# Kernel tuning notes

Measured on AMD Instinct MI355X. Metric: run time of the kernel, lower is better.

The kernel has to match this reference:

```python
import jax, jax.numpy as jnp
import numpy as np

B, S, D, DS = 8, 2048, 1024, 128
TEMP = 1.0
C = 8.0


def setup_inputs() -> dict:
    key = jax.random.key(0)
    ks = jax.random.split(key, 8)
    s_in = 1.0 / np.sqrt(D)
    s_st = 1.0 / np.sqrt(DS)
    return {
        "x": jax.random.normal(ks[0], (B, S, D), jnp.float32),
        "W_k": jax.random.normal(ks[1], (DS, D), jnp.float32) * s_in,
        "W_v": jax.random.normal(ks[2], (DS, D), jnp.float32) * s_in,
        "W_q": jax.random.normal(ks[3], (DS, D), jnp.float32) * s_in,
        "W_alpha_w": jax.random.normal(ks[4], (DS, D), jnp.float32) * s_in,
        "W_alpha_b": jnp.zeros((DS,), jnp.float32),
        "lambda_param": jax.random.uniform(ks[5], (DS,), jnp.float32, 4.0, 9.0),
        "W_o": jax.random.normal(ks[6], (D, DS), jnp.float32) * s_st,
        "norm_weight": jnp.ones((DS,), jnp.float32),
    }


def _l2norm(z):
    # matches F.normalize(..., dim=-1) with eps=1e-12
    n = jnp.linalg.norm(z, axis=-1, keepdims=True)
    return z / jnp.maximum(n, 1e-12)


def reference(x, W_k, W_v, W_q, W_alpha_w, W_alpha_b, lambda_param, W_o, norm_weight):
    # projections
    k = _l2norm(x @ W_k.T)                      # [B,S,DS]
    v = x @ W_v.T                               # [B,S,DS]
    q = _l2norm(x @ W_q.T)                      # [B,S,DS]
    r = jax.nn.sigmoid(x @ W_alpha_w.T + W_alpha_b)
    log_a = jnp.log(jax.nn.sigmoid(lambda_param) + 1e-8)  # [DS]
    alpha = jnp.exp(C * r * log_a)              # [B,S,DS], data-dependent decay

    H0 = jnp.zeros((B, DS, DS), x.dtype)        # state indexed [b, k, v]

    def step(H, inp):
        k_t, v_t, q_t, a_t = inp                # each [B,DS]
        # surprise: prediction error against current state
        pred = jnp.einsum('bk,bkv->bv', q_t, H)
        err = jnp.sum((v_t - pred) ** 2, axis=-1, keepdims=True)  # [B,1]
        sur = jax.nn.sigmoid(err / (TEMP + 1e-6))                 # [B,1]
        # delta rule: k (x) v - k (x) (k^T H) = k (x) (v - k^T H)
        k_proj = jnp.einsum('bk,bkv->bv', k_t, H)
        delta = k_t[:, :, None] * (v_t - k_proj)[:, None, :]      # [B,DS,DS]
        a_e = a_t[:, :, None]                                     # decay on k-axis
        H = a_e * H + (1.0 - a_e) * (sur[:, :, None] * delta)
        y = jnp.einsum('bk,bkv->bv', q_t, H)
        return H, y

    seq = (k.transpose(1, 0, 2), v.transpose(1, 0, 2),
           q.transpose(1, 0, 2), alpha.transpose(1, 0, 2))
    _, ys = jax.lax.scan(step, H0, seq)         # ys: [S,B,DS]
    y = ys.transpose(1, 0, 2)                   # [B,S,DS]

    # RMSNorm (computed in fp32, like the torch module)
    yf = y.astype(jnp.float32)
    yn = yf * jax.lax.rsqrt(jnp.mean(yf * yf, axis=-1, keepdims=True) + 1e-6)
    yn = (yn * norm_weight).astype(y.dtype)
    return yn @ W_o.T                           # [B,S,D]
```

## Files before the change

### kernel.cpp

```cpp
#include <hip/hip_runtime.h>
#include <math.h>

#define S_LEN 2048
#define B_SZ 8
#define D_IN 1024
#define DS_ 128
#define INV_TEMP (1.0f/1.000001f)

__global__ __launch_bounds__(256) void proj_gemm(
    const float* __restrict__ X,
    const float* __restrict__ Wk, const float* __restrict__ Wv,
    const float* __restrict__ Wq, const float* __restrict__ Wa,
    float* __restrict__ P)
{
    __shared__ __align__(16) float As[32][68];
    __shared__ __align__(16) float Bs[32][68];
    const int tid = threadIdx.x;
    const int m0 = blockIdx.x * 64;
    const int n0 = blockIdx.y * 64;
    const int lr = tid >> 3;
    const int lk4 = tid & 7;

    const float* wrows[2];
#pragma unroll
    for (int i = 0; i < 2; i++) {
        int nn = n0 + lr + i * 32;
        const float* w;
        if      (nn < 128) w = Wk + (size_t)nn * D_IN;
        else if (nn < 256) w = Wv + (size_t)(nn - 128) * D_IN;
        else if (nn < 384) w = Wq + (size_t)(nn - 256) * D_IN;
        else               w = Wa + (size_t)(nn - 384) * D_IN;
        wrows[i] = w;
    }
    const int ty = tid >> 4, tx = tid & 15;
    float acc[4][4];
#pragma unroll
    for (int i = 0; i < 4; i++)
#pragma unroll
        for (int j = 0; j < 4; j++) acc[i][j] = 0.f;

    for (int k0 = 0; k0 < D_IN; k0 += 32) {
#pragma unroll
        for (int i = 0; i < 2; i++) {
            int m = lr + i * 32;
            float4 a4 = *(const float4*)(X + (size_t)(m0 + m) * D_IN + k0 + lk4 * 4);
            As[lk4*4+0][m] = a4.x; As[lk4*4+1][m] = a4.y;
            As[lk4*4+2][m] = a4.z; As[lk4*4+3][m] = a4.w;
            float4 b4 = *(const float4*)(wrows[i] + k0 + lk4 * 4);
            Bs[lk4*4+0][m] = b4.x; Bs[lk4*4+1][m] = b4.y;
            Bs[lk4*4+2][m] = b4.z; Bs[lk4*4+3][m] = b4.w;
        }
        __syncthreads();
#pragma unroll
        for (int kk = 0; kk < 32; kk++) {
            float4 a4 = *(const float4*)(&As[kk][ty * 4]);
            float4 b4 = *(const float4*)(&Bs[kk][tx * 4]);
            float a[4] = {a4.x, a4.y, a4.z, a4.w};
            float b[4] = {b4.x, b4.y, b4.z, b4.w};
#pragma unroll
            for (int i = 0; i < 4; i++)
#pragma unroll
                for (int j = 0; j < 4; j++)
                    acc[i][j] = fmaf(a[i], b[j], acc[i][j]);
        }
        __syncthreads();
    }
#pragma unroll
    for (int i = 0; i < 4; i++) {
        float4 o; o.x = acc[i][0]; o.y = acc[i][1]; o.z = acc[i][2]; o.w = acc[i][3];
        *(float4*)(P + (size_t)(m0 + ty * 4 + i) * 512 + n0 + tx * 4) = o;
    }
}

__global__ __launch_bounds__(128) void postproc(
    float* __restrict__ P, const float* __restrict__ bA, const float* __restrict__ lam)
{
    const int tok = blockIdx.x, i = threadIdx.x;
    float* row = P + (size_t)tok * 512;
    float kr = row[i], qr = row[256 + i], rr = row[384 + i];
    float ks = kr * kr, qs = qr * qr;
#pragma unroll
    for (int m = 1; m < 64; m <<= 1) { ks += __shfl_xor(ks, m); qs += __shfl_xor(qs, m); }
    __shared__ float sb[4];
    if ((i & 63) == 0) { sb[(i >> 6) * 2] = ks; sb[(i >> 6) * 2 + 1] = qs; }
    __syncthreads();
    float kn = sqrtf(sb[0] + sb[2]);
    float qn = sqrtf(sb[1] + sb[3]);
    float kinv = 1.0f / fmaxf(kn, 1e-12f);
    float qinv = 1.0f / fmaxf(qn, 1e-12f);
    float sr = 1.0f / (1.0f + __expf(-(rr + bA[i])));
    float sl = 1.0f / (1.0f + __expf(-lam[i]));
    float la = logf(sl + 1e-8f);
    row[i]       = kr * kinv;
    row[256 + i] = qr * qinv;
    row[384 + i] = __expf(8.0f * sr * la);
}

__global__ __launch_bounds__(256) void recurrence(
    const float* __restrict__ P, float* __restrict__ Y)
{
    const int b = blockIdx.x;
    const int tid = threadIdx.x;
    const int c = tid & 3;
    const int vp = tid >> 2;
    const int lane = tid & 63;
    const int wave = tid >> 6;

    __shared__ __align__(16) float Pbuf[3][576];
    __shared__ float errw[2][4];

    const float* Pb = P + (size_t)b * S_LEN * 512;
    float* Yb = Y + (size_t)b * S_LEN * DS_;

    float H0[32], H1[32];
#pragma unroll
    for (int j = 0; j < 32; j++) { H0[j] = 0.f; H1[j] = 0.f; }

    for (int i = tid; i < 3 * 576; i += 256) (&Pbuf[0][0])[i] = 0.f;
    __syncthreads();
    {
        float2 v2 = *(const float2*)(Pb + tid * 2);
        int i0 = tid * 2, i1 = i0 + 1;
        Pbuf[0][(i0 >> 7) * 144 + ((i0 >> 5) & 3) * 36 + (i0 & 31)] = v2.x;
        Pbuf[0][(i1 >> 7) * 144 + ((i1 >> 5) & 3) * 36 + (i1 & 31)] = v2.y;
    }
    __syncthreads();

    const int voff = 144 + (vp >> 4) * 36 + ((2 * vp) & 31);

#define DOT_STEP(u, comp) { float h0 = H0[j4*4+u], h1 = H1[j4*4+u]; \
    pr0 = fmaf(q4.comp, h0, pr0); pr1 = fmaf(q4.comp, h1, pr1); \
    kp0 = fmaf(k4.comp, h0, kp0); kp1 = fmaf(k4.comp, h1, kp1); \
    yp0 = fmaf(p4.comp, h0, yp0); yp1 = fmaf(p4.comp, h1, yp1); }

#define UPD_STEP(u, comp) { float t0 = k4.comp * sd0, t1 = k4.comp * sd1; \
    H0[j4*4+u] = fmaf(a4.comp, H0[j4*4+u] - t0, t0); \
    H1[j4*4+u] = fmaf(a4.comp, H1[j4*4+u] - t1, t1); }

    for (int t = 0; t < S_LEN; t++) {
        const int pc = t % 3, pn = (t + 1) % 3, pp = (t + 2) % 3;
        const float* bq = &Pbuf[pc][2 * 144 + c * 36];
        const float* bk = &Pbuf[pc][c * 36];
        const float* bp = &Pbuf[pp][2 * 144 + c * 36];
        float pr0 = 0, pr1 = 0, kp0 = 0, kp1 = 0, yp0 = 0, yp1 = 0;
#pragma unroll
        for (int j4 = 0; j4 < 8; j4++) {
            float4 q4 = *(const float4*)(bq + j4 * 4);
            float4 k4 = *(const float4*)(bk + j4 * 4);
            float4 p4 = *(const float4*)(bp + j4 * 4);
            DOT_STEP(0, x) DOT_STEP(1, y) DOT_STEP(2, z) DOT_STEP(3, w)
        }
#pragma unroll
        for (int m = 1; m <= 2; m <<= 1) {
            pr0 += __shfl_xor(pr0, m); pr1 += __shfl_xor(pr1, m);
            kp0 += __shfl_xor(kp0, m); kp1 += __shfl_xor(kp1, m);
            yp0 += __shfl_xor(yp0, m); yp1 += __shfl_xor(yp1, m);
        }
        float2 vt = *(const float2*)(&Pbuf[pc][voff]);
        float e0 = vt.x - pr0, e1 = vt.y - pr1;
        float d0 = vt.x - kp0, d1 = vt.y - kp1;
        float ep = e0 * e0 + e1 * e1;
        ep += __shfl_xor(ep, 4); ep += __shfl_xor(ep, 8);
        ep += __shfl_xor(ep, 16); ep += __shfl_xor(ep, 32);
        if (lane == 0) errw[t & 1][wave] = ep * 0.25f;
        if (t > 0 && c == 0) {
            float2 yv; yv.x = yp0; yv.y = yp1;
            *(float2*)(Yb + (size_t)(t - 1) * DS_ + vp * 2) = yv;
        }
        if (t + 1 < S_LEN) {
            float2 v2 = *(const float2*)(Pb + (size_t)(t + 1) * 512 + tid * 2);
            int i0 = tid * 2, i1 = i0 + 1;
            Pbuf[pn][(i0 >> 7) * 144 + ((i0 >> 5) & 3) * 36 + (i0 & 31)] = v2.x;
            Pbuf[pn][(i1 >> 7) * 144 + ((i1 >> 5) & 3) * 36 + (i1 & 31)] = v2.y;
        }
        __syncthreads();
        float err = errw[t & 1][0] + errw[t & 1][1] + errw[t & 1][2] + errw[t & 1][3];
        float sur = 1.0f / (1.0f + __expf(-err * INV_TEMP));
        float sd0 = sur * d0, sd1 = sur * d1;
        const float* ba = &Pbuf[pc][3 * 144 + c * 36];
#pragma unroll
        for (int j4 = 0; j4 < 8; j4++) {
            float4 a4 = *(const float4*)(ba + j4 * 4);
            float4 k4 = *(const float4*)(bk + j4 * 4);
            UPD_STEP(0, x) UPD_STEP(1, y) UPD_STEP(2, z) UPD_STEP(3, w)
        }
    }
    {
        const float* bq = &Pbuf[(S_LEN - 1) % 3][2 * 144 + c * 36];
        float y0 = 0, y1 = 0;
#pragma unroll
        for (int j4 = 0; j4 < 8; j4++) {
            float4 q4 = *(const float4*)(bq + j4 * 4);
            y0 = fmaf(q4.x, H0[j4*4+0], y0); y1 = fmaf(q4.x, H1[j4*4+0], y1);
            y0 = fmaf(q4.y, H0[j4*4+1], y0); y1 = fmaf(q4.y, H1[j4*4+1], y1);
            y0 = fmaf(q4.z, H0[j4*4+2], y0); y1 = fmaf(q4.z, H1[j4*4+2], y1);
            y0 = fmaf(q4.w, H0[j4*4+3], y0); y1 = fmaf(q4.w, H1[j4*4+3], y1);
        }
        y0 += __shfl_xor(y0, 1); y0 += __shfl_xor(y0, 2);
        y1 += __shfl_xor(y1, 1); y1 += __shfl_xor(y1, 2);
        if (c == 0) {
            float2 yv; yv.x = y0; yv.y = y1;
            *(float2*)(Yb + (size_t)(S_LEN - 1) * DS_ + vp * 2) = yv;
        }
    }
#undef DOT_STEP
#undef UPD_STEP
}

__global__ __launch_bounds__(128) void rmsnorm(
    const float* __restrict__ Y, const float* __restrict__ nw, float* __restrict__ Yn)
{
    const int tok = blockIdx.x, i = threadIdx.x;
    float y = Y[(size_t)tok * DS_ + i];
    float s = y * y;
#pragma unroll
    for (int m = 1; m < 64; m <<= 1) s += __shfl_xor(s, m);
    __shared__ float sb[2];
    if ((i & 63) == 0) sb[i >> 6] = s;
    __syncthreads();
    float ms = (sb[0] + sb[1]) * (1.0f / 128.0f);
    Yn[(size_t)tok * DS_ + i] = y * rsqrtf(ms + 1e-6f) * nw[i];
}

__global__ __launch_bounds__(256) void out_gemm(
    const float* __restrict__ Yn, const float* __restrict__ Wo, float* __restrict__ Out)
{
    __shared__ __align__(16) float As[32][68];
    __shared__ __align__(16) float Bs[32][68];
    const int tid = threadIdx.x;
    const int m0 = blockIdx.x * 64;
    const int n0 = blockIdx.y * 64;
    const int lr = tid >> 3;
    const int lk4 = tid & 7;
    const int ty = tid >> 4, tx = tid & 15;
    float acc[4][4];
#pragma unroll
    for (int i = 0; i < 4; i++)
#pragma unroll
        for (int j = 0; j < 4; j++) acc[i][j] = 0.f;

    for (int k0 = 0; k0 < DS_; k0 += 32) {
#pragma unroll
        for (int i = 0; i < 2; i++) {
            int m = lr + i * 32;
            float4 a4 = *(const float4*)(Yn + (size_t)(m0 + m) * DS_ + k0 + lk4 * 4);
            As[lk4*4+0][m] = a4.x; As[lk4*4+1][m] = a4.y;
            As[lk4*4+2][m] = a4.z; As[lk4*4+3][m] = a4.w;
            float4 b4 = *(const float4*)(Wo + (size_t)(n0 + m) * DS_ + k0 + lk4 * 4);
            Bs[lk4*4+0][m] = b4.x; Bs[lk4*4+1][m] = b4.y;
            Bs[lk4*4+2][m] = b4.z; Bs[lk4*4+3][m] = b4.w;
        }
        __syncthreads();
#pragma unroll
        for (int kk = 0; kk < 32; kk++) {
            float4 a4 = *(const float4*)(&As[kk][ty * 4]);
            float4 b4 = *(const float4*)(&Bs[kk][tx * 4]);
            float a[4] = {a4.x, a4.y, a4.z, a4.w};
            float b[4] = {b4.x, b4.y, b4.z, b4.w};
#pragma unroll
            for (int i = 0; i < 4; i++)
#pragma unroll
                for (int j = 0; j < 4; j++)
                    acc[i][j] = fmaf(a[i], b[j], acc[i][j]);
        }
        __syncthreads();
    }
#pragma unroll
    for (int i = 0; i < 4; i++) {
        float4 o; o.x = acc[i][0]; o.y = acc[i][1]; o.z = acc[i][2]; o.w = acc[i][3];
        *(float4*)(Out + (size_t)(m0 + ty * 4 + i) * 1024 + n0 + tx * 4) = o;
    }
}

extern "C" void kernel_launch(void* const* d_in, const int* in_sizes, int n_in,
                              void* d_out, int out_size, void* d_ws, size_t ws_size,
                              hipStream_t stream)
{
    const float* x   = (const float*)d_in[0];
    const float* Wk  = (const float*)d_in[1];
    const float* Wv  = (const float*)d_in[2];
    const float* Wq  = (const float*)d_in[3];
    const float* Waw = (const float*)d_in[4];
    const float* Wab = (const float*)d_in[5];
    const float* lam = (const float*)d_in[6];
    const float* Wo  = (const float*)d_in[7];
    const float* nw  = (const float*)d_in[8];
    float* out = (float*)d_out;

    const size_t NTOK = (size_t)B_SZ * S_LEN;
    float* P  = (float*)d_ws;
    float* Y  = P + NTOK * 512;
    float* Yn = Y + NTOK * DS_;

    proj_gemm<<<dim3(NTOK / 64, 512 / 64), 256, 0, stream>>>(x, Wk, Wv, Wq, Waw, P);
    postproc<<<NTOK, 128, 0, stream>>>(P, Wab, lam);
    recurrence<<<B_SZ, 256, 0, stream>>>(P, Y);
    rmsnorm<<<NTOK, 128, 0, stream>>>(Y, nw, Yn);
    out_gemm<<<dim3(NTOK / 64, 1024 / 64), 256, 0, stream>>>(Yn, Wo, out);
}
```

Baseline: 3.216 ms.

## Compute recurrence output algebraically from pre-update state, widen to 512 threads

The recurrence now derives y_t from the pre-update state: y = (q*a)·H + sur*g*(v - k^T H), where g = sum(q*(1-a)*k) is precomputed per token in postproc. This removes the one-step-lagged third dot product against the previous buffer. The block grows to 512 threads with 8 lanes per value pair, halving per-thread state registers. Global loads are software-pipelined two steps ahead through registers, and the step loop is unrolled by two. The cost is an extra reduction in postproc, an extra workspace buffer, and more shuffle stages per step.

```diff
diff --git a/kernel.cpp b/kernel.cpp
--- a/kernel.cpp
+++ b/kernel.cpp
@@ -73,7 +73,8 @@
 }
 
 __global__ __launch_bounds__(128) void postproc(
-    float* __restrict__ P, const float* __restrict__ bA, const float* __restrict__ lam)
+    float* __restrict__ P, float* __restrict__ G,
+    const float* __restrict__ bA, const float* __restrict__ lam)
 {
     const int tok = blockIdx.x, i = threadIdx.x;
     float* row = P + (size_t)tok * 512;
@@ -81,130 +82,130 @@
     float ks = kr * kr, qs = qr * qr;
 #pragma unroll
     for (int m = 1; m < 64; m <<= 1) { ks += __shfl_xor(ks, m); qs += __shfl_xor(qs, m); }
-    __shared__ float sb[4];
+    __shared__ float sb[6];
     if ((i & 63) == 0) { sb[(i >> 6) * 2] = ks; sb[(i >> 6) * 2 + 1] = qs; }
     __syncthreads();
-    float kn = sqrtf(sb[0] + sb[2]);
-    float qn = sqrtf(sb[1] + sb[3]);
-    float kinv = 1.0f / fmaxf(kn, 1e-12f);
-    float qinv = 1.0f / fmaxf(qn, 1e-12f);
+    float kinv = 1.0f / fmaxf(sqrtf(sb[0] + sb[2]), 1e-12f);
+    float qinv = 1.0f / fmaxf(sqrtf(sb[1] + sb[3]), 1e-12f);
+    float kn = kr * kinv, qn = qr * qinv;
     float sr = 1.0f / (1.0f + __expf(-(rr + bA[i])));
     float sl = 1.0f / (1.0f + __expf(-lam[i]));
     float la = logf(sl + 1e-8f);
-    row[i]       = kr * kinv;
-    row[256 + i] = qr * qinv;
-    row[384 + i] = __expf(8.0f * sr * la);
-}
-
-__global__ __launch_bounds__(256) void recurrence(
-    const float* __restrict__ P, float* __restrict__ Y)
+    float al = __expf(8.0f * sr * la);
+    row[i]       = kn;
+    row[256 + i] = qn;
+    row[384 + i] = al;
+    float gi = qn * (1.0f - al) * kn;
+#pragma unroll
+    for (int m = 1; m < 64; m <<= 1) gi += __shfl_xor(gi, m);
+    if ((i & 63) == 0) sb[4 + (i >> 6)] = gi;
+    __syncthreads();
+    if (i == 0) G[tok] = sb[4] + sb[5];
+}
+
+__global__ __launch_bounds__(512, 2) void recurrence(
+    const float* __restrict__ P, const float* __restrict__ G, float* __restrict__ Y)
 {
     const int b = blockIdx.x;
     const int tid = threadIdx.x;
-    const int c = tid & 3;
-    const int vp = tid >> 2;
+    const int c = tid & 7;
+    const int vp = tid >> 3;
     const int lane = tid & 63;
     const int wave = tid >> 6;
 
-    __shared__ __align__(16) float Pbuf[3][576];
-    __shared__ float errw[2][4];
+    __shared__ __align__(16) float Pbuf[3][808];
+    __shared__ __align__(16) float errw[2][8];
 
     const float* Pb = P + (size_t)b * S_LEN * 512;
+    const float* Gb = G + (size_t)b * S_LEN;
     float* Yb = Y + (size_t)b * S_LEN * DS_;
 
-    float H0[32], H1[32];
-#pragma unroll
-    for (int j = 0; j < 32; j++) { H0[j] = 0.f; H1[j] = 0.f; }
-
-    for (int i = tid; i < 3 * 576; i += 256) (&Pbuf[0][0])[i] = 0.f;
+    float H0[16], H1[16];
+#pragma unroll
+    for (int j = 0; j < 16; j++) { H0[j] = 0.f; H1[j] = 0.f; }
+
+    const bool isP = tid < 256;
+    const bool isG = (tid == 256);
+    int spos = 0;
+    if (isP) {
+        int i0 = tid * 2, sec = i0 >> 7, idx = i0 & 127;
+        spos = sec * 160 + (idx >> 4) * 20 + (idx & 15);
+    }
+    const int voff = 160 + (vp >> 3) * 20 + ((2 * vp) & 15);
+
+    float2 rp0, rp1; float rg0 = 0.f, rg1 = 0.f;
+    if (isP) {
+        rp0 = *(const float2*)(Pb + tid * 2);
+        rp1 = *(const float2*)(Pb + 512 + tid * 2);
+    }
+    if (isG) { rg0 = Gb[0]; rg1 = Gb[1]; }
+    if (isP) *(float2*)(&Pbuf[0][spos]) = rp0;
+    if (isG) Pbuf[0][800] = rg0;
     __syncthreads();
-    {
-        float2 v2 = *(const float2*)(Pb + tid * 2);
-        int i0 = tid * 2, i1 = i0 + 1;
-        Pbuf[0][(i0 >> 7) * 144 + ((i0 >> 5) & 3) * 36 + (i0 & 31)] = v2.x;
-        Pbuf[0][(i1 >> 7) * 144 + ((i1 >> 5) & 3) * 36 + (i1 & 31)] = v2.y;
-    }
-    __syncthreads();
-
-    const int voff = 144 + (vp >> 4) * 36 + ((2 * vp) & 31);
-
-#define DOT_STEP(u, comp) { float h0 = H0[j4*4+u], h1 = H1[j4*4+u]; \
-    pr0 = fmaf(q4.comp, h0, pr0); pr1 = fmaf(q4.comp, h1, pr1); \
-    kp0 = fmaf(k4.comp, h0, kp0); kp1 = fmaf(k4.comp, h1, kp1); \
-    yp0 = fmaf(p4.comp, h0, yp0); yp1 = fmaf(p4.comp, h1, yp1); }
-
-#define UPD_STEP(u, comp) { float t0 = k4.comp * sd0, t1 = k4.comp * sd1; \
-    H0[j4*4+u] = fmaf(a4.comp, H0[j4*4+u] - t0, t0); \
-    H1[j4*4+u] = fmaf(a4.comp, H1[j4*4+u] - t1, t1); }
-
-    for (int t = 0; t < S_LEN; t++) {
-        const int pc = t % 3, pn = (t + 1) % 3, pp = (t + 2) % 3;
-        const float* bq = &Pbuf[pc][2 * 144 + c * 36];
-        const float* bk = &Pbuf[pc][c * 36];
-        const float* bp = &Pbuf[pp][2 * 144 + c * 36];
-        float pr0 = 0, pr1 = 0, kp0 = 0, kp1 = 0, yp0 = 0, yp1 = 0;
-#pragma unroll
-        for (int j4 = 0; j4 < 8; j4++) {
-            float4 q4 = *(const float4*)(bq + j4 * 4);
-            float4 k4 = *(const float4*)(bk + j4 * 4);
-            float4 p4 = *(const float4*)(bp + j4 * 4);
-            DOT_STEP(0, x) DOT_STEP(1, y) DOT_STEP(2, z) DOT_STEP(3, w)
-        }
-#pragma unroll
-        for (int m = 1; m <= 2; m <<= 1) {
-            pr0 += __shfl_xor(pr0, m); pr1 += __shfl_xor(pr1, m);
-            kp0 += __shfl_xor(kp0, m); kp1 += __shfl_xor(kp1, m);
-            yp0 += __shfl_xor(yp0, m); yp1 += __shfl_xor(yp1, m);
-        }
-        float2 vt = *(const float2*)(&Pbuf[pc][voff]);
-        float e0 = vt.x - pr0, e1 = vt.y - pr1;
-        float d0 = vt.x - kp0, d1 = vt.y - kp1;
-        float ep = e0 * e0 + e1 * e1;
-        ep += __shfl_xor(ep, 4); ep += __shfl_xor(ep, 8);
-        ep += __shfl_xor(ep, 16); ep += __shfl_xor(ep, 32);
-        if (lane == 0) errw[t & 1][wave] = ep * 0.25f;
-        if (t > 0 && c == 0) {
-            float2 yv; yv.x = yp0; yv.y = yp1;
-            *(float2*)(Yb + (size_t)(t - 1) * DS_ + vp * 2) = yv;
-        }
-        if (t + 1 < S_LEN) {
-            float2 v2 = *(const float2*)(Pb + (size_t)(t + 1) * 512 + tid * 2);
-            int i0 = tid * 2, i1 = i0 + 1;
-            Pbuf[pn][(i0 >> 7) * 144 + ((i0 >> 5) & 3) * 36 + (i0 & 31)] = v2.x;
-            Pbuf[pn][(i1 >> 7) * 144 + ((i1 >> 5) & 3) * 36 + (i1 & 31)] = v2.y;
-        }
-        __syncthreads();
-        float err = errw[t & 1][0] + errw[t & 1][1] + errw[t & 1][2] + errw[t & 1][3];
-        float sur = 1.0f / (1.0f + __expf(-err * INV_TEMP));
-        float sd0 = sur * d0, sd1 = sur * d1;
-        const float* ba = &Pbuf[pc][3 * 144 + c * 36];
-#pragma unroll
-        for (int j4 = 0; j4 < 8; j4++) {
-            float4 a4 = *(const float4*)(ba + j4 * 4);
-            float4 k4 = *(const float4*)(bk + j4 * 4);
-            UPD_STEP(0, x) UPD_STEP(1, y) UPD_STEP(2, z) UPD_STEP(3, w)
-        }
-    }
-    {
-        const float* bq = &Pbuf[(S_LEN - 1) % 3][2 * 144 + c * 36];
-        float y0 = 0, y1 = 0;
-#pragma unroll
-        for (int j4 = 0; j4 < 8; j4++) {
-            float4 q4 = *(const float4*)(bq + j4 * 4);
-            y0 = fmaf(q4.x, H0[j4*4+0], y0); y1 = fmaf(q4.x, H1[j4*4+0], y1);
-            y0 = fmaf(q4.y, H0[j4*4+1], y0); y1 = fmaf(q4.y, H1[j4*4+1], y1);
-            y0 = fmaf(q4.z, H0[j4*4+2], y0); y1 = fmaf(q4.z, H1[j4*4+2], y1);
-            y0 = fmaf(q4.w, H0[j4*4+3], y0); y1 = fmaf(q4.w, H1[j4*4+3], y1);
-        }
-        y0 += __shfl_xor(y0, 1); y0 += __shfl_xor(y0, 2);
-        y1 += __shfl_xor(y1, 1); y1 += __shfl_xor(y1, 2);
-        if (c == 0) {
-            float2 yv; yv.x = y0; yv.y = y1;
-            *(float2*)(Yb + (size_t)(S_LEN - 1) * DS_ + vp * 2) = yv;
-        }
-    }
-#undef DOT_STEP
-#undef UPD_STEP
+
+#define DOTC(j, u, comp) { \
+    float q_ = q4[j].comp, k_ = k4[j].comp, a_ = a4[j].comp; \
+    float h0 = H0[(j)*4+(u)], h1 = H1[(j)*4+(u)]; \
+    pr0 = fmaf(q_, h0, pr0); pr1 = fmaf(q_, h1, pr1); \
+    kp0 = fmaf(k_, h0, kp0); kp1 = fmaf(k_, h1, kp1); \
+    float qa_ = q_ * a_; \
+    ya0 = fmaf(qa_, h0, ya0); ya1 = fmaf(qa_, h1, ya1); }
+
+#define UPDC(j, u, comp) { \
+    float k_ = k4[j].comp, a_ = a4[j].comp; \
+    float t0 = k_ * sd0, t1 = k_ * sd1; \
+    H0[(j)*4+(u)] = fmaf(a_, H0[(j)*4+(u)] - t0, t0); \
+    H1[(j)*4+(u)] = fmaf(a_, H1[(j)*4+(u)] - t1, t1); }
+
+#define STEP(T, PAR, RPS, RGS, RPL, RGL) { \
+    float* cb = &Pbuf[(T) % 3][0]; \
+    const float* bk = cb + c * 20; \
+    float4 k4[4], q4[4], a4[4]; \
+    _Pragma("unroll") for (int j = 0; j < 4; j++) { \
+        k4[j] = *(const float4*)(bk + j * 4); \
+        q4[j] = *(const float4*)(bk + 320 + j * 4); \
+        a4[j] = *(const float4*)(bk + 480 + j * 4); } \
+    float2 vt = *(const float2*)(cb + voff); \
+    float g = cb[800]; \
+    float pr0 = 0, pr1 = 0, kp0 = 0, kp1 = 0, ya0 = 0, ya1 = 0; \
+    _Pragma("unroll") for (int j = 0; j < 4; j++) { \
+        DOTC(j, 0, x) DOTC(j, 1, y) DOTC(j, 2, z) DOTC(j, 3, w) } \
+    _Pragma("unroll") for (int m = 1; m <= 4; m <<= 1) { \
+        pr0 += __shfl_xor(pr0, m); pr1 += __shfl_xor(pr1, m); \
+        kp0 += __shfl_xor(kp0, m); kp1 += __shfl_xor(kp1, m); \
+        ya0 += __shfl_xor(ya0, m); ya1 += __shfl_xor(ya1, m); } \
+    float e0 = vt.x - pr0, e1 = vt.y - pr1; \
+    float d0 = vt.x - kp0, d1 = vt.y - kp1; \
+    float ep = fmaf(e0, e0, e1 * e1); \
+    ep += __shfl_xor(ep, 8); ep += __shfl_xor(ep, 16); ep += __shfl_xor(ep, 32); \
+    if (lane == 0) errw[PAR][wave] = ep; \
+    if ((T) + 1 < S_LEN) { \
+        if (isP) *(float2*)(&Pbuf[((T) + 1) % 3][spos]) = RPS; \
+        if (isG) Pbuf[((T) + 1) % 3][800] = RGS; } \
+    if ((T) + 2 < S_LEN) { \
+        if (isP) RPL = *(const float2*)(Pb + (size_t)((T) + 2) * 512 + tid * 2); \
+        if (isG) RGL = Gb[(T) + 2]; } \
+    __syncthreads(); \
+    float4 ea = *(const float4*)(&errw[PAR][0]); \
+    float4 eb = *(const float4*)(&errw[PAR][4]); \
+    float err = ((ea.x + ea.y) + (ea.z + ea.w)) + ((eb.x + eb.y) + (eb.z + eb.w)); \
+    float sur = 1.0f / (1.0f + __expf(-err * INV_TEMP)); \
+    float sd0 = sur * d0, sd1 = sur * d1; \
+    if (c == 0) { \
+        float2 yv; float sg = sur * g; \
+        yv.x = fmaf(sg, d0, ya0); yv.y = fmaf(sg, d1, ya1); \
+        *(float2*)(Yb + (size_t)(T) * DS_ + vp * 2) = yv; } \
+    _Pragma("unroll") for (int j = 0; j < 4; j++) { \
+        UPDC(j, 0, x) UPDC(j, 1, y) UPDC(j, 2, z) UPDC(j, 3, w) } \
+}
+
+    for (int t = 0; t < S_LEN; t += 2) {
+        STEP(t,     0, rp1, rg1, rp0, rg0)
+        STEP(t + 1, 1, rp0, rg0, rp1, rg1)
+    }
+#undef DOTC
+#undef UPDC
+#undef STEP
 }
 
 __global__ __launch_bounds__(128) void rmsnorm(
@@ -291,10 +292,11 @@
     float* P  = (float*)d_ws;
     float* Y  = P + NTOK * 512;
     float* Yn = Y + NTOK * DS_;
+    float* G  = Yn + NTOK * DS_;
 
     proj_gemm<<<dim3(NTOK / 64, 512 / 64), 256, 0, stream>>>(x, Wk, Wv, Wq, Waw, P);
-    postproc<<<NTOK, 128, 0, stream>>>(P, Wab, lam);
-    recurrence<<<B_SZ, 256, 0, stream>>>(P, Y);
+    postproc<<<NTOK, 128, 0, stream>>>(P, G, Wab, lam);
+    recurrence<<<B_SZ, 512, 0, stream>>>(P, G, Y);
     rmsnorm<<<NTOK, 128, 0, stream>>>(Y, nw, Yn);
     out_gemm<<<dim3(NTOK / 64, 1024 / 64), 256, 0, stream>>>(Yn, Wo, out);
 }
```

After: 3.003 ms. -6.6%, faster.
